# Optimization experiments

Measured on AMD Instinct MI355X. Metric: run time of the kernel, lower is better.

Reference implementation:

```python
import jax, jax.numpy as jnp
import numpy as np

PENALTY = -100.0  # reset penalty used by the torch module


def log_g(x):
    # torch: where(x >= 0, log(relu(x) + 0.5), -softplus(-x))
    return jnp.where(x >= 0, jnp.log(jax.nn.relu(x) + 0.5), -jax.nn.softplus(-x))


def setup_inputs() -> dict:
    key = jax.random.key(0)
    k1, k2, k3 = jax.random.split(key, 3)
    B, S, D = 4, 8192, 1024
    x = jax.random.normal(k1, (B, S, D), dtype=jnp.float32)
    W = jax.random.normal(k2, (D, 2 * D), dtype=jnp.float32) * (1.0 / np.sqrt(D))
    input_ids = jax.random.randint(k3, (B, S), 0, 32000, dtype=jnp.int64)
    return {"x": x, "W": W, "input_ids": input_ids}


def reference(x, W, input_ids):
    # x: [B,S,D], W: [D,2D] (to_hidden_and_gate, no bias), proj_out=False -> Identity
    hg = jnp.einsum("bsd,de->bse", x, W)            # [B,S,2D]
    hidden, gate = jnp.split(hg, 2, axis=-1)          # each [B,S,D]

    pad_mask = input_ids == 0                         # [B,S]

    log_coeffs = -jax.nn.softplus(gate)               # log(1 - z)
    log_z = -jax.nn.softplus(-gate)                   # log z
    log_values = log_z + log_g(hidden)                # log(z * h_tilde)

    # reset at positions following a pad token (shifted mask)
    reset = jnp.pad(pad_mask[:, :-1], ((0, 0), (1, 0)))[:, :, None]  # [B,S,1]

    lc = jnp.where(reset, PENALTY, log_coeffs)
    a_star = jnp.cumsum(lc, axis=1)
    lv = jnp.where(reset, PENALTY, log_values)
    log_h = a_star + jax.lax.cumlogsumexp(lv - a_star, axis=1)
    out = jnp.exp(log_h)                              # [B,S,D]

    next_prev_hidden = jnp.where(pad_mask[:, -1:, None], 0.0, out[:, -1:])
    return out, next_prev_hidden
```

## Files before the change

kernel.cpp:

```cpp
#include <hip/hip_runtime.h>
#include <hip/hip_fp16.h>
#include <math.h>

#define S_LEN 8192
#define D_DIM 1024
#define B_DIM 4
#define M_DIM (B_DIM * S_LEN)
#define BSD   ((size_t)M_DIM * D_DIM)
#define CHN   (B_DIM * D_DIM)
#define CHUNK 64
#define NCH   (S_LEN / CHUNK)

typedef _Float16 f16x8 __attribute__((ext_vector_type(8)));
typedef __attribute__((ext_vector_type(4))) float f32x4;
typedef unsigned int u32;

__device__ __forceinline__ u32 pk2h(float a, float b) {
    auto h = __builtin_amdgcn_cvt_pkrtz(a, b);
    u32 r; __builtin_memcpy(&r, &h, 4); return r;
}

__device__ __forceinline__ void gload16(const void* g, void* l) {
    __builtin_amdgcn_global_load_lds(
        (const __attribute__((address_space(1))) u32*)g,
        (__attribute__((address_space(3))) u32*)l,
        16, 0, 0);
}

__global__ __launch_bounds__(256) void w_to_f16t(
    const float* __restrict__ W, unsigned short* __restrict__ Wt)
{
    __shared__ float T[64][65];
    const int t  = threadIdx.x;
    const int n0 = (int)blockIdx.x * 64;
    const int k0 = (int)blockIdx.y * 64;
    #pragma unroll
    for (int p = 0; p < 4; ++p) {
        int u = p * 256 + t;
        int r = u >> 4, c4 = (u & 15) * 4;
        float4 v = *(const float4*)&W[(size_t)(k0 + r) * 2048 + n0 + c4];
        T[r][c4 + 0] = v.x; T[r][c4 + 1] = v.y;
        T[r][c4 + 2] = v.z; T[r][c4 + 3] = v.w;
    }
    __syncthreads();
    #pragma unroll
    for (int p = 0; p < 2; ++p) {
        int u = p * 256 + t;
        int n = u >> 3, kc = (u & 7) * 8;
        u32 out[4];
        #pragma unroll
        for (int j = 0; j < 4; ++j)
            out[j] = pk2h(T[kc + 2 * j][n], T[kc + 2 * j + 1][n]);
        *(uint4*)&Wt[(size_t)(n0 + n) * 1024 + k0 + kc] = *(uint4*)out;
    }
}

__global__ __launch_bounds__(256) void x_to_f16sw(
    const float* __restrict__ x, unsigned short* __restrict__ xh)
{
    int tid = (int)blockIdx.x * 256 + threadIdx.x;
    int m  = tid >> 7;
    int cg = tid & 127;
    const float4* src = (const float4*)&x[(size_t)m * 1024 + cg * 8];
    float4 v0 = src[0], v1 = src[1];
    u32 o[4] = { pk2h(v0.x, v0.y), pk2h(v0.z, v0.w),
                 pk2h(v1.x, v1.y), pk2h(v1.z, v1.w) };
    int j   = cg & 7;
    int cgd = (cg & ~7) | (j ^ (m & 7));
    *(uint4*)&xh[(size_t)m * 1024 + cgd * 8] = *(uint4*)o;
}

__global__ __launch_bounds__(512, 2) void gemm_8p(
    const unsigned short* __restrict__ xh, const unsigned short* __restrict__ Wt,
    const int* __restrict__ ids, u32* __restrict__ P)
{
    __shared__ __align__(16) unsigned short Ah[2 * 256 * 64];
    __shared__ __align__(16) unsigned short Bt[2 * 256 * 64];

    const int t    = threadIdx.x;
    const int lane = t & 63;
    const int wid  = t >> 6;
    const int wm   = wid >> 2;
    const int wd   = wid & 3;

    const int lin  = (int)blockIdx.x;
    const int xcd  = lin & 7;
    const int slot = lin >> 3;
    const int m0   = (xcd * 16 + (slot >> 3)) * 256;
    const int c0   = (slot & 7) * 128;

    f32x4 accH[8][2], accG[8][2];
    #pragma unroll
    for (int i = 0; i < 8; ++i)
        #pragma unroll
        for (int j = 0; j < 2; ++j) {
            accH[i][j] = (f32x4)0.0f;
            accG[i][j] = (f32x4)0.0f;
        }

    auto stageA = [&](int kb, int buf, int half) {
        char* Ad = (char*)Ah + (buf << 15) + (half << 14);
        #pragma unroll
        for (int i = 0; i < 2; ++i) {
            int sl  = i * 512 + t;
            int row = half * 128 + (sl >> 3);
            int c   = sl & 7;
            const unsigned short* src =
                xh + ((size_t)(m0 + row) << 10) + kb + (c << 3);
            gload16(src, Ad + (size_t)sl * 16);
        }
    };
    auto stageB = [&](int kb, int buf, int half) {
        char* Bd = (char*)Bt + (buf << 15) + (half << 14);
        #pragma unroll
        for (int i = 0; i < 2; ++i) {
            int sl  = i * 512 + t;
            int col = sl >> 3;
            int kc  = (sl & 7) ^ (col & 7);
            const unsigned short* src =
                Wt + ((size_t)(half * 1024 + c0 + col) << 10) + kb + (kc << 3);
            gload16(src, Bd + (size_t)sl * 16);
        }
    };

    auto readA = [&](const char* Ab, int kk, f16x8 a[8]) {
        int chunk = kk * 4 + (lane >> 4);
        #pragma unroll
        for (int mf = 0; mf < 8; ++mf) {
            int row = wm * 128 + mf * 16 + (lane & 15);
            a[mf] = *(const f16x8*)(Ab + row * 128 + ((chunk ^ (row & 7)) << 4));
        }
    };
    auto readB = [&](const char* Bb, int kk, int hg, f16x8 b[2]) {
        int chunk = kk * 4 + (lane >> 4);
        #pragma unroll
        for (int df = 0; df < 2; ++df) {
            int col = wd * 32 + df * 16 + (lane & 15);
            b[df] = *(const f16x8*)(Bb + (hg * 128 + col) * 128
                                       + ((chunk ^ (col & 7)) << 4));
        }
    };

    #define MMA_CLUSTER(ACC)                                               \
        __builtin_amdgcn_s_setprio(1);                                     \
        _Pragma("unroll")                                                  \
        for (int mf = 0; mf < 8; ++mf)                                     \
            _Pragma("unroll")                                              \
            for (int df = 0; df < 2; ++df)                                 \
                ACC[mf][df] = __builtin_amdgcn_mfma_f32_16x16x32_f16(      \
                    a[mf], b[df], ACC[mf][df], 0, 0, 0);                   \
        __builtin_amdgcn_s_setprio(0);

    stageA(0, 0, 0); stageA(0, 0, 1); stageB(0, 0, 0); stageB(0, 0, 1);
    asm volatile("s_waitcnt vmcnt(2)" ::: "memory");
    __builtin_amdgcn_sched_barrier(0);
    __builtin_amdgcn_s_barrier();

    for (int tt = 0; tt < 16; ++tt) {
        const int buf  = tt & 1;
        const int kbn  = (tt + 1) << 6;
        const bool more = tt < 15;
        const char* Ab = (const char*)Ah + (buf << 15);
        const char* Bb = (const char*)Bt + (buf << 15);
        f16x8 a[8], b[2];

        readA(Ab, 0, a); readB(Bb, 0, 0, b);
        if (more) stageA(kbn, buf ^ 1, 0);
        __builtin_amdgcn_s_barrier();
        asm volatile("s_waitcnt lgkmcnt(0)" ::: "memory");
        __builtin_amdgcn_sched_barrier(0);
        MMA_CLUSTER(accH)
        if (more) asm volatile("s_waitcnt vmcnt(2)" ::: "memory");
        else      asm volatile("s_waitcnt vmcnt(0)" ::: "memory");
        __builtin_amdgcn_sched_barrier(0);
        __builtin_amdgcn_s_barrier();

        readB(Bb, 0, 1, b);
        if (more) stageA(kbn, buf ^ 1, 1);
        __builtin_amdgcn_s_barrier();
        asm volatile("s_waitcnt lgkmcnt(0)" ::: "memory");
        __builtin_amdgcn_sched_barrier(0);
        MMA_CLUSTER(accG)
        __builtin_amdgcn_s_barrier();

        readA(Ab, 1, a); readB(Bb, 1, 0, b);
        if (more) stageB(kbn, buf ^ 1, 0);
        __builtin_amdgcn_s_barrier();
        asm volatile("s_waitcnt lgkmcnt(0)" ::: "memory");
        __builtin_amdgcn_sched_barrier(0);
        MMA_CLUSTER(accH)
        __builtin_amdgcn_s_barrier();

        readB(Bb, 1, 1, b);
        if (more) stageB(kbn, buf ^ 1, 1);
        __builtin_amdgcn_s_barrier();
        asm volatile("s_waitcnt lgkmcnt(0)" ::: "memory");
        __builtin_amdgcn_sched_barrier(0);
        MMA_CLUSTER(accG)
        if (more) {
            asm volatile("s_waitcnt vmcnt(2)" ::: "memory");
        }
        __builtin_amdgcn_sched_barrier(0);
        __builtin_amdgcn_s_barrier();
    }
    #undef MMA_CLUSTER

    #pragma unroll
    for (int mf = 0; mf < 8; ++mf) {
        int mbase = m0 + wm * 128 + mf * 16 + (lane >> 4) * 4;
        #pragma unroll
        for (int r = 0; r < 4; ++r) {
            int m = mbase + r;
            int b = m >> 13;
            int s = m & 8191;
            bool reset = (s > 0) && (ids[b * S_LEN + s - 1] == 0);
            #pragma unroll
            for (int df = 0; df < 2; ++df) {
                int d = c0 + wd * 32 + df * 16 + (lane & 15);
                float hid = accH[mf][df][r];
                float g   = accG[mf][df][r];
                float eg  = __expf(-g);
                float z   = 1.0f / (1.0f + eg);
                float c   = eg * z;
                float gt  = (hid >= 0.0f) ? (hid + 0.5f)
                                          : 1.0f / (1.0f + __expf(-hid));
                float v   = z * gt;
                if (reset) { c = 0.0f; v = 0.0f; }
                __half2 h2 = __floats2half2_rn(c, v);
                u32 packed;
                __builtin_memcpy(&packed, &h2, 4);
                P[(size_t)m * D_DIM + d] = packed;
            }
        }
    }
}

__global__ __launch_bounds__(256, 3) void gemm_fb(
    const float* __restrict__ x, const unsigned short* __restrict__ Wt,
    const int* __restrict__ ids, u32* __restrict__ P)
{
    __shared__ __align__(16) unsigned short Ah[128 * 64];
    __shared__ __align__(16) unsigned short Bt[2 * 64 * 64];

    const int t    = threadIdx.x;
    const int lane = t & 63;
    const int wid  = t >> 6;
    const int wm   = wid >> 1;
    const int wd   = wid & 1;

    const int lin  = (int)blockIdx.y * (int)gridDim.x + (int)blockIdx.x;
    const int xcd  = lin & 7;
    const int slot = lin >> 3;
    const int m0   = (xcd * 32 + (slot >> 4)) * 128;
    const int c0   = (slot & 15) * 64;

    f32x4 accH[4][2], accG[4][2];
    #pragma unroll
    for (int i = 0; i < 4; ++i)
        #pragma unroll
        for (int j = 0; j < 2; ++j) {
            accH[i][j] = (f32x4)0.0f;
            accG[i][j] = (f32x4)0.0f;
        }

    for (int kb = 0; kb < 1024; kb += 64) {
        __syncthreads();
        #pragma unroll
        for (int i = 0; i < 4; ++i) {
            int slotb = wid * 256 + i * 64;
            int sl  = slotb + lane;
            int hg  = sl >> 9;
            int col = (sl >> 3) & 63;
            int kc  = (sl & 7) ^ (col & 7);
            const unsigned short* src =
                Wt + ((size_t)(hg * 1024 + c0 + col) << 10) + kb + (kc << 3);
            gload16(src, (char*)Bt + (size_t)slotb * 16);
        }
        #pragma unroll
        for (int p = 0; p < 8; ++p) {
            int s   = p * 256 + t;
            int row = s >> 4;
            int c4  = s & 15;
            float4 v = *(const float4*)&x[(size_t)(m0 + row) * 1024 + kb + c4 * 4];
            uint2 h;
            h.x = pk2h(v.x, v.y);
            h.y = pk2h(v.z, v.w);
            int byte = row * 128 + ((((c4 >> 1) ^ (row & 7))) << 4) + ((c4 & 1) << 3);
            *(uint2*)((char*)Ah + byte) = h;
        }
        __syncthreads();
        #pragma unroll
        for (int kk = 0; kk < 2; ++kk) {
            f16x8 bh[2], bg[2];
            #pragma unroll
            for (int df = 0; df < 2; ++df) {
                int col = wd * 32 + df * 16 + (lane & 15);
                int chunk = kk * 4 + (lane >> 4);
                int byte = col * 128 + ((chunk ^ (col & 7)) << 4);
                bh[df] = *(const f16x8*)((const char*)Bt + byte);
                bg[df] = *(const f16x8*)((const char*)Bt + 8192 + byte);
            }
            #pragma unroll
            for (int mf = 0; mf < 4; ++mf) {
                int row = wm * 64 + mf * 16 + (lane & 15);
                int chunk = kk * 4 + (lane >> 4);
                int byte = row * 128 + ((chunk ^ (row & 7)) << 4);
                f16x8 a = *(const f16x8*)((const char*)Ah + byte);
                #pragma unroll
                for (int df = 0; df < 2; ++df) {
                    accH[mf][df] = __builtin_amdgcn_mfma_f32_16x16x32_f16(
                        a, bh[df], accH[mf][df], 0, 0, 0);
                    accG[mf][df] = __builtin_amdgcn_mfma_f32_16x16x32_f16(
                        a, bg[df], accG[mf][df], 0, 0, 0);
                }
            }
        }
    }

    #pragma unroll
    for (int mf = 0; mf < 4; ++mf) {
        int mbase = m0 + wm * 64 + mf * 16 + (lane >> 4) * 4;
        #pragma unroll
        for (int r = 0; r < 4; ++r) {
            int m = mbase + r;
            int b = m >> 13;
            int s = m & 8191;
            bool reset = (s > 0) && (ids[b * S_LEN + s - 1] == 0);
            #pragma unroll
            for (int df = 0; df < 2; ++df) {
                int d = c0 + wd * 32 + df * 16 + (lane & 15);
                float hid = accH[mf][df][r];
                float g   = accG[mf][df][r];
                float eg  = __expf(-g);
                float z   = 1.0f / (1.0f + eg);
                float c   = eg * z;
                float gt  = (hid >= 0.0f) ? (hid + 0.5f)
                                          : 1.0f / (1.0f + __expf(-hid));
                float v   = z * gt;
                if (reset) { c = 0.0f; v = 0.0f; }
                __half2 h2 = __floats2half2_rn(c, v);
                u32 packed;
                __builtin_memcpy(&packed, &h2, 4);
                P[(size_t)m * D_DIM + d] = packed;
            }
        }
    }
}

__global__ __launch_bounds__(256) void scan_phase_a(
    const u32* __restrict__ P,
    float* __restrict__ Cp, float* __restrict__ Lp)
{
    int ch0 = (blockIdx.x * 256 + threadIdx.x) * 4;
    int c   = blockIdx.y;
    int b   = ch0 >> 10;
    int d0  = ch0 & 1023;
    size_t base = (size_t)b * S_LEN * D_DIM + d0;
    int s0 = c * CHUNK;

    float C[4] = {1.f, 1.f, 1.f, 1.f};
    float H[4] = {0.f, 0.f, 0.f, 0.f};
    for (int s = 0; s < CHUNK; ++s) {
        uint4 q = *(const uint4*)&P[base + (size_t)(s0 + s) * D_DIM];
        u32 qs[4] = {q.x, q.y, q.z, q.w};
        #pragma unroll
        for (int j = 0; j < 4; ++j) {
            __half2 h2;
            __builtin_memcpy(&h2, &qs[j], 4);
            float cc = __low2float(h2);
            float vv = __high2float(h2);
            H[j] = fmaf(cc, H[j], vv);
            C[j] *= cc;
        }
    }
    *(float4*)&Cp[c * CHN + ch0] = *(float4*)C;
    *(float4*)&Lp[c * CHN + ch0] = *(float4*)H;
}

__global__ __launch_bounds__(256) void scan_phase_b(
    const float* __restrict__ Cp, const float* __restrict__ Lp,
    float* __restrict__ carry)
{
    int ch = blockIdx.x * 256 + threadIdx.x;
    float h = 0.0f;
    for (int c = 0; c < NCH; ++c) {
        carry[c * CHN + ch] = h;
        h = fmaf(Cp[c * CHN + ch], h, Lp[c * CHN + ch]);
    }
}

__global__ __launch_bounds__(256) void scan_phase_c(
    u32* __restrict__ Pio,
    const float* __restrict__ carry,
    const int* __restrict__ ids)
{
    int ch0 = (blockIdx.x * 256 + threadIdx.x) * 4;
    int c   = blockIdx.y;
    int b   = ch0 >> 10;
    int d0  = ch0 & 1023;
    size_t base = (size_t)b * S_LEN * D_DIM + d0;
    int s0 = c * CHUNK;

    float H[4];
    *(float4*)H = *(const float4*)&carry[c * CHN + ch0];

    for (int s = 0; s < CHUNK; ++s) {
        size_t idx = base + (size_t)(s0 + s) * D_DIM;
        uint4 q = *(const uint4*)&Pio[idx];
        u32 qs[4] = {q.x, q.y, q.z, q.w};
        u32 os[4];
        #pragma unroll
        for (int j = 0; j < 4; ++j) {
            __half2 h2;
            __builtin_memcpy(&h2, &qs[j], 4);
            float cc = __low2float(h2);
            float vv = __high2float(h2);
            H[j] = fmaf(cc, H[j], vv);
            os[j] = __float_as_uint(H[j]);
        }
        *(uint4*)&Pio[idx] = *(uint4*)os;
    }
    if (c == NCH - 1) {
        bool pad = (ids[b * S_LEN + (S_LEN - 1)] == 0);
        u32 os[4];
        #pragma unroll
        for (int j = 0; j < 4; ++j)
            os[j] = __float_as_uint(pad ? 0.0f : H[j]);
        *(uint4*)&Pio[BSD + (size_t)b * D_DIM + d0] = *(uint4*)os;
    }
}

extern "C" void kernel_launch(void* const* d_in, const int* in_sizes, int n_in,
                              void* d_out, int out_size, void* d_ws, size_t ws_size,
                              hipStream_t stream) {
    const float* x   = (const float*)d_in[0];
    const float* W   = (const float*)d_in[1];
    const int*   ids = (const int*)d_in[2];

    u32* P = (u32*)d_out;
    unsigned short* Wt = (unsigned short*)d_ws;
    float* Cp    = (float*)((char*)d_ws + (size_t) 4 * 1024 * 1024);
    float* Lp    = (float*)((char*)d_ws + (size_t) 6 * 1024 * 1024);
    float* carry = (float*)((char*)d_ws + (size_t) 8 * 1024 * 1024);
    unsigned short* xh = (unsigned short*)((char*)d_ws + (size_t)10 * 1024 * 1024);
    const size_t need = (size_t)10 * 1024 * 1024 + BSD * 2;

    w_to_f16t<<<dim3(32, 16), 256, 0, stream>>>(W, Wt);

    if (ws_size >= need) {
        x_to_f16sw<<<(M_DIM * 128) / 256, 256, 0, stream>>>(x, xh);
        gemm_8p<<<1024, 512, 0, stream>>>(xh, Wt, ids, P);
    } else {
        dim3 ggrid(D_DIM / 64, M_DIM / 128);
        gemm_fb<<<ggrid, 256, 0, stream>>>(x, Wt, ids, P);
    }

    dim3 sgrid(CHN / 1024, NCH);
    scan_phase_a<<<sgrid, 256, 0, stream>>>(P, Cp, Lp);
    scan_phase_b<<<CHN / 256, 256, 0, stream>>>(Cp, Lp, carry);
    scan_phase_c<<<sgrid, 256, 0, stream>>>(P, carry, ids);
}
```

Measured before the change: 277.1 us.

## Double-buffer register fragments to overlap LDS reads with MFMA clusters

Restructures the GEMM main loop so LDS fragment reads for the next MFMA cluster are issued before the current cluster runs, using separate register sets for each A/B fragment. Most intra-iteration workgroup barriers are removed, leaving one barrier per K-step after a full vmcnt(0) wait. Global-to-LDS staging of A and B halves is issued in pairs. This raises register pressure and uses full vmcnt waits in place of partial ones, which could expose global load latency or reduce occupancy.

```diff
diff --git a/kernel.cpp b/kernel.cpp
--- a/kernel.cpp
+++ b/kernel.cpp
@@ -141,67 +141,58 @@
         }
     };
 
-    #define MMA_CLUSTER(ACC)                                               \
+    #define MMA_CLUSTER(ACC, AV, BV)                                       \
         __builtin_amdgcn_s_setprio(1);                                     \
         _Pragma("unroll")                                                  \
         for (int mf = 0; mf < 8; ++mf)                                     \
             _Pragma("unroll")                                              \
             for (int df = 0; df < 2; ++df)                                 \
                 ACC[mf][df] = __builtin_amdgcn_mfma_f32_16x16x32_f16(      \
-                    a[mf], b[df], ACC[mf][df], 0, 0, 0);                   \
+                    AV[mf], BV[df], ACC[mf][df], 0, 0, 0);                 \
         __builtin_amdgcn_s_setprio(0);
 
     stageA(0, 0, 0); stageA(0, 0, 1); stageB(0, 0, 0); stageB(0, 0, 1);
-    asm volatile("s_waitcnt vmcnt(2)" ::: "memory");
+    asm volatile("s_waitcnt vmcnt(0)" ::: "memory");
     __builtin_amdgcn_sched_barrier(0);
     __builtin_amdgcn_s_barrier();
 
     for (int tt = 0; tt < 16; ++tt) {
-        const int buf  = tt & 1;
-        const int kbn  = (tt + 1) << 6;
+        const int buf   = tt & 1;
+        const int kbn   = (tt + 1) << 6;
         const bool more = tt < 15;
         const char* Ab = (const char*)Ah + (buf << 15);
         const char* Bb = (const char*)Bt + (buf << 15);
-        f16x8 a[8], b[2];
-
-        readA(Ab, 0, a); readB(Bb, 0, 0, b);
-        if (more) stageA(kbn, buf ^ 1, 0);
-        __builtin_amdgcn_s_barrier();
+        f16x8 a0[8], a1[8], bh0[2], bg0[2], bh1[2], bg1[2];
+
+        readA(Ab, 0, a0); readB(Bb, 0, 0, bh0);
+        if (more) { stageA(kbn, buf ^ 1, 0); stageA(kbn, buf ^ 1, 1); }
         asm volatile("s_waitcnt lgkmcnt(0)" ::: "memory");
         __builtin_amdgcn_sched_barrier(0);
-        MMA_CLUSTER(accH)
-        if (more) asm volatile("s_waitcnt vmcnt(2)" ::: "memory");
-        else      asm volatile("s_waitcnt vmcnt(0)" ::: "memory");
-        __builtin_amdgcn_sched_barrier(0);
-        __builtin_amdgcn_s_barrier();
-
-        readB(Bb, 0, 1, b);
-        if (more) stageA(kbn, buf ^ 1, 1);
-        __builtin_amdgcn_s_barrier();
+        readB(Bb, 0, 1, bg0);
+        __builtin_amdgcn_sched_barrier(0);
+        MMA_CLUSTER(accH, a0, bh0)
+
         asm volatile("s_waitcnt lgkmcnt(0)" ::: "memory");
         __builtin_amdgcn_sched_barrier(0);
-        MMA_CLUSTER(accG)
-        __builtin_amdgcn_s_barrier();
-
-        readA(Ab, 1, a); readB(Bb, 1, 0, b);
-        if (more) stageB(kbn, buf ^ 1, 0);
-        __builtin_amdgcn_s_barrier();
+        readA(Ab, 1, a1); readB(Bb, 1, 0, bh1);
+        if (more) { stageB(kbn, buf ^ 1, 0); stageB(kbn, buf ^ 1, 1); }
+        __builtin_amdgcn_sched_barrier(0);
+        MMA_CLUSTER(accG, a0, bg0)
+
         asm volatile("s_waitcnt lgkmcnt(0)" ::: "memory");
         __builtin_amdgcn_sched_barrier(0);
-        MMA_CLUSTER(accH)
-        __builtin_amdgcn_s_barrier();
-
-        readB(Bb, 1, 1, b);
-        if (more) stageB(kbn, buf ^ 1, 1);
-        __builtin_amdgcn_s_barrier();
+        readB(Bb, 1, 1, bg1);
+        __builtin_amdgcn_sched_barrier(0);
+        MMA_CLUSTER(accH, a1, bh1)
+
         asm volatile("s_waitcnt lgkmcnt(0)" ::: "memory");
         __builtin_amdgcn_sched_barrier(0);
-        MMA_CLUSTER(accG)
+        MMA_CLUSTER(accG, a1, bg1)
         if (more) {
-            asm volatile("s_waitcnt vmcnt(2)" ::: "memory");
-        }
-        __builtin_amdgcn_sched_barrier(0);
-        __builtin_amdgcn_s_barrier();
+            asm volatile("s_waitcnt vmcnt(0)" ::: "memory");
+            __builtin_amdgcn_sched_barrier(0);
+            __builtin_amdgcn_s_barrier();
+        }
     }
     #undef MMA_CLUSTER
 
```

After: 272.6 us. About the same (-1.6%).
